# Optimization experiments

Measured on AMD Instinct MI355X. Metric: run time of the kernel, lower is better.

## Reference

```python
import jax, jax.numpy as jnp
import numpy as np

N_USERS, N_ITEMS, P, F = 100000, 200000, 8, 64
B, S = 4096, 200

def setup_inputs() -> dict:
    key = jax.random.key(0)
    k1, k2, k3, k4 = jax.random.split(key, 4)
    user = jax.random.randint(k1, (B,), 0, N_USERS)
    items = jax.random.randint(k2, (B, S), 0, N_ITEMS)
    # xavier_normal init: std = sqrt(2/(fan_in+fan_out)) per torch semantics on last two dims
    std_u = np.sqrt(2.0 / (P + F))
    std_i = np.sqrt(2.0 / (N_ITEMS + F))
    user_factors = jax.random.normal(k3, (N_USERS, P, F), dtype=jnp.float32) * std_u
    item_factors = jax.random.normal(k4, (N_ITEMS, F), dtype=jnp.float32) * std_i
    return {"user": user, "items": items, "user_factors": user_factors, "item_factors": item_factors}

def reference(user, items, user_factors, item_factors):
    u = user_factors[user]          # [B, P, F]
    v = item_factors[items]         # [B, S, F]
    r = jnp.einsum('bsf,bpf->bsp', v, u)            # [B, S, P]
    attentive_scores = jax.nn.softmax(r, axis=-1)   # softmax over personas
    attentive_user = jnp.einsum('bpf,bsp->bsf', u, attentive_scores)  # [B, S, F]
    pred = jnp.einsum('bsf,bsf->bs', attentive_user, v)               # [B, S]
    return (pred, attentive_scores)
```

## Files before the change

kernel.cpp:

```cpp
#include <hip/hip_runtime.h>

#define NB 4096
#define NS 200
#define NP 8
#define NF 64

#define RB 5
#define LPS 50
#define IT 4

__global__ __launch_bounds__(256) void cf_kernel(
    const int*   __restrict__ user,
    const int*   __restrict__ items,
    const float* __restrict__ user_factors,
    const float* __restrict__ item_factors,
    float* __restrict__ out_pred,
    float* __restrict__ out_scores)
{
    __shared__ float u_lds[RB][NF * NP];

    const int tid  = threadIdx.x;
    const int b0   = blockIdx.x * RB;
    const int rows = min(RB, NB - b0);

    for (int e = tid; e < rows * (NP * NF); e += 256) {
        int g = e >> 9;
        int q = e & 511;
        int uid = user[b0 + g];
        float w = user_factors[(size_t)uid * (NP * NF) + q];
        int p = q >> 6, f = q & 63;
        u_lds[g][f * NP + p] = w;
    }
    __syncthreads();

    const int g = tid / LPS;
    const int l = tid - g * LPS;
    if (g >= rows) return;
    const int b = b0 + g;
    const float* __restrict__ ug = u_lds[g];

    const float4* vp[IT];
    int svec[IT];
    #pragma unroll
    for (int k = 0; k < IT; ++k) {
        int s = l + LPS * k;
        svec[k] = s;
        int idx = items[b * NS + s];
        vp[k] = (const float4*)(item_factors + (size_t)idx * NF);
    }

    float acc[IT][NP];
    #pragma unroll
    for (int k = 0; k < IT; ++k)
        #pragma unroll
        for (int p = 0; p < NP; ++p) acc[k][p] = 0.f;

    #pragma unroll
    for (int c = 0; c < NF / 8; ++c) {
        float4 v[IT][2];
        #pragma unroll
        for (int k = 0; k < IT; ++k) {
            v[k][0] = vp[k][2 * c];
            v[k][1] = vp[k][2 * c + 1];
        }
        #pragma unroll
        for (int j = 0; j < 8; ++j) {
            const float4* up = (const float4*)&ug[(c * 8 + j) * NP];
            float4 ua = up[0];
            float4 ub = up[1];
            #pragma unroll
            for (int k = 0; k < IT; ++k) {
                float vv = ((const float*)&v[k][0])[j];
                acc[k][0] += vv * ua.x;  acc[k][1] += vv * ua.y;
                acc[k][2] += vv * ua.z;  acc[k][3] += vv * ua.w;
                acc[k][4] += vv * ub.x;  acc[k][5] += vv * ub.y;
                acc[k][6] += vv * ub.z;  acc[k][7] += vv * ub.w;
            }
        }
    }

    #pragma unroll
    for (int k = 0; k < IT; ++k) {
        float m = acc[k][0];
        #pragma unroll
        for (int p = 1; p < NP; ++p) m = fmaxf(m, acc[k][p]);
        float e[NP], sum = 0.f;
        #pragma unroll
        for (int p = 0; p < NP; ++p) { e[p] = __expf(acc[k][p] - m); sum += e[p]; }
        float inv = 1.f / sum;

        float sc[NP], pred = 0.f;
        #pragma unroll
        for (int p = 0; p < NP; ++p) {
            sc[p] = e[p] * inv;
            pred += sc[p] * acc[k][p];
        }

        const int s = svec[k];
        out_pred[b * NS + s] = pred;
        float4* op = (float4*)(out_scores + (size_t)(b * NS + s) * NP);
        op[0] = make_float4(sc[0], sc[1], sc[2], sc[3]);
        op[1] = make_float4(sc[4], sc[5], sc[6], sc[7]);
    }
}

extern "C" void kernel_launch(void* const* d_in, const int* in_sizes, int n_in,
                              void* d_out, int out_size, void* d_ws, size_t ws_size,
                              hipStream_t stream) {
    const int*   user         = (const int*)d_in[0];
    const int*   items        = (const int*)d_in[1];
    const float* user_factors = (const float*)d_in[2];
    const float* item_factors = (const float*)d_in[3];

    float* out_pred   = (float*)d_out;
    float* out_scores = out_pred + (size_t)NB * NS;

    const int grid = (NB + RB - 1) / RB;
    cf_kernel<<<grid, 256, 0, stream>>>(user, items, user_factors, item_factors,
                                        out_pred, out_scores);
}
```

Measured before the change: 346.4 us.

## Prefetch full item rows for two sequence positions per pass

Each thread now handles its four sequence positions as two passes of two items. Per pass it loads both full 64-float item rows up front, 32 float4 values in registers, rather than interleaving 8-float chunks of four rows with the FMA loop. This issues more bytes of gather loads back to back per item to improve memory-level parallelism. The cost is fewer items in flight at once and higher register pressure, which may lower occupancy.

```diff
diff --git a/kernel.cpp b/kernel.cpp
--- a/kernel.cpp
+++ b/kernel.cpp
@@ -7,7 +7,6 @@
 
 #define RB 5
 #define LPS 50
-#define IT 4
 
 __global__ __launch_bounds__(256) void cf_kernel(
     const int*   __restrict__ user,
@@ -39,68 +38,69 @@
     const int b = b0 + g;
     const float* __restrict__ ug = u_lds[g];
 
-    const float4* vp[IT];
-    int svec[IT];
     #pragma unroll
-    for (int k = 0; k < IT; ++k) {
-        int s = l + LPS * k;
-        svec[k] = s;
-        int idx = items[b * NS + s];
-        vp[k] = (const float4*)(item_factors + (size_t)idx * NF);
-    }
+    for (int half = 0; half < 2; ++half) {
+        const int s0 = l + LPS * (2 * half);
+        const int s1 = s0 + LPS;
+        const int i0 = items[b * NS + s0];
+        const int i1 = items[b * NS + s1];
+        const float4* p0 = (const float4*)(item_factors + (size_t)i0 * NF);
+        const float4* p1 = (const float4*)(item_factors + (size_t)i1 * NF);
 
-    float acc[IT][NP];
-    #pragma unroll
-    for (int k = 0; k < IT; ++k)
+        float4 v0[16], v1[16];
         #pragma unroll
-        for (int p = 0; p < NP; ++p) acc[k][p] = 0.f;
+        for (int i = 0; i < 16; ++i) v0[i] = p0[i];
+        #pragma unroll
+        for (int i = 0; i < 16; ++i) v1[i] = p1[i];
 
-    #pragma unroll
-    for (int c = 0; c < NF / 8; ++c) {
-        float4 v[IT][2];
+        float a0[NP], a1[NP];
         #pragma unroll
-        for (int k = 0; k < IT; ++k) {
-            v[k][0] = vp[k][2 * c];
-            v[k][1] = vp[k][2 * c + 1];
-        }
+        for (int p = 0; p < NP; ++p) { a0[p] = 0.f; a1[p] = 0.f; }
+
         #pragma unroll
-        for (int j = 0; j < 8; ++j) {
-            const float4* up = (const float4*)&ug[(c * 8 + j) * NP];
-            float4 ua = up[0];
-            float4 ub = up[1];
+        for (int c = 0; c < 8; ++c) {
             #pragma unroll
-            for (int k = 0; k < IT; ++k) {
-                float vv = ((const float*)&v[k][0])[j];
-                acc[k][0] += vv * ua.x;  acc[k][1] += vv * ua.y;
-                acc[k][2] += vv * ua.z;  acc[k][3] += vv * ua.w;
-                acc[k][4] += vv * ub.x;  acc[k][5] += vv * ub.y;
-                acc[k][6] += vv * ub.z;  acc[k][7] += vv * ub.w;
+            for (int j = 0; j < 8; ++j) {
+                const float4* up = (const float4*)&ug[(c * 8 + j) * NP];
+                float4 ua = up[0];
+                float4 ub = up[1];
+                float x0 = ((const float*)&v0[2 * c])[j];
+                float x1 = ((const float*)&v1[2 * c])[j];
+                a0[0] += x0 * ua.x;  a0[1] += x0 * ua.y;
+                a0[2] += x0 * ua.z;  a0[3] += x0 * ua.w;
+                a0[4] += x0 * ub.x;  a0[5] += x0 * ub.y;
+                a0[6] += x0 * ub.z;  a0[7] += x0 * ub.w;
+                a1[0] += x1 * ua.x;  a1[1] += x1 * ua.y;
+                a1[2] += x1 * ua.z;  a1[3] += x1 * ua.w;
+                a1[4] += x1 * ub.x;  a1[5] += x1 * ub.y;
+                a1[6] += x1 * ub.z;  a1[7] += x1 * ub.w;
             }
         }
-    }
 
-    #pragma unroll
-    for (int k = 0; k < IT; ++k) {
-        float m = acc[k][0];
         #pragma unroll
-        for (int p = 1; p < NP; ++p) m = fmaxf(m, acc[k][p]);
-        float e[NP], sum = 0.f;
-        #pragma unroll
-        for (int p = 0; p < NP; ++p) { e[p] = __expf(acc[k][p] - m); sum += e[p]; }
-        float inv = 1.f / sum;
+        for (int which = 0; which < 2; ++which) {
+            float* a = which ? a1 : a0;
+            const int s = which ? s1 : s0;
+            float m = a[0];
+            #pragma unroll
+            for (int p = 1; p < NP; ++p) m = fmaxf(m, a[p]);
+            float e[NP], sum = 0.f;
+            #pragma unroll
+            for (int p = 0; p < NP; ++p) { e[p] = __expf(a[p] - m); sum += e[p]; }
+            float inv = 1.f / sum;
 
-        float sc[NP], pred = 0.f;
-        #pragma unroll
-        for (int p = 0; p < NP; ++p) {
-            sc[p] = e[p] * inv;
-            pred += sc[p] * acc[k][p];
+            float sc[NP], pred = 0.f;
+            #pragma unroll
+            for (int p = 0; p < NP; ++p) {
+                sc[p] = e[p] * inv;
+                pred += sc[p] * a[p];
+            }
+
+            out_pred[b * NS + s] = pred;
+            float4* op = (float4*)(out_scores + (size_t)(b * NS + s) * NP);
+            op[0] = make_float4(sc[0], sc[1], sc[2], sc[3]);
+            op[1] = make_float4(sc[4], sc[5], sc[6], sc[7]);
         }
-
-        const int s = svec[k];
-        out_pred[b * NS + s] = pred;
-        float4* op = (float4*)(out_scores + (size_t)(b * NS + s) * NP);
-        op[0] = make_float4(sc[0], sc[1], sc[2], sc[3]);
-        op[1] = make_float4(sc[4], sc[5], sc[6], sc[7]);
     }
 }
 
```

Result: slower. 499.1 us (+44.1%).
